# Kernel optimization log

Measured on AMD Instinct MI355X. Metric: run time of the kernel, lower is better.

Reference implementation:

```python
import jax, jax.numpy as jnp
import numpy as np
from jax import lax

B, IN_CH, OUT_CH, H, W = 32, 128, 256, 64, 64
STYLE_CH, TDIM, G = 512, 512, 32
GN_EPS, MOD_EPS = 1e-5, 1e-8
DN = ('NCHW', 'OIHW', 'NCHW')


def swish(x):
    return x * jax.nn.sigmoid(x)


def group_norm(x, gamma, beta):
    n, c, h, w = x.shape
    xr = x.reshape(n, G, c // G, h, w)
    mu = xr.mean(axis=(2, 3, 4), keepdims=True)
    var = xr.var(axis=(2, 3, 4), keepdims=True)
    xn = ((xr - mu) * lax.rsqrt(var + GN_EPS)).reshape(n, c, h, w)
    return xn * gamma[None, :, None, None] + beta[None, :, None, None]


def conv3x3(x, w, b):
    y = lax.conv_general_dilated(x, w, (1, 1), ((1, 1), (1, 1)), dimension_numbers=DN)
    return y + b[None, :, None, None]


def setup_inputs() -> dict:
    key = jax.random.key(0)
    ks = jax.random.split(key, 16)
    s = 0.05
    return {
        'x': jax.random.normal(ks[0], (B, IN_CH, H, W), jnp.float32),
        'temb': jax.random.normal(ks[1], (B, TDIM), jnp.float32),
        'style': jax.random.normal(ks[2], (B, STYLE_CH), jnp.float32),
        'gn1_g': jnp.ones((IN_CH,), jnp.float32),
        'gn1_b': jnp.zeros((IN_CH,), jnp.float32),
        'conv1_w': jax.random.normal(ks[3], (OUT_CH, IN_CH, 3, 3), jnp.float32) * s,
        'conv1_b': jnp.zeros((OUT_CH,), jnp.float32),
        'temb_w': jax.random.normal(ks[4], (OUT_CH, TDIM), jnp.float32) * s,
        'temb_b': jnp.zeros((OUT_CH,), jnp.float32),
        'gn2_g': jnp.ones((OUT_CH,), jnp.float32),
        'gn2_b': jnp.zeros((OUT_CH,), jnp.float32),
        'style_w': jax.random.normal(ks[5], (OUT_CH, STYLE_CH), jnp.float32) * s,
        'style_b': jnp.zeros((OUT_CH,), jnp.float32),
        'mod_w': jax.random.normal(ks[6], (OUT_CH, OUT_CH, 3, 3), jnp.float32) * s,
        'sc_w': jax.random.normal(ks[7], (OUT_CH, IN_CH, 1, 1), jnp.float32) * s,
        'sc_b': jnp.zeros((OUT_CH,), jnp.float32),
    }


def reference(x, temb, style, gn1_g, gn1_b, conv1_w, conv1_b, temb_w, temb_b,
              gn2_g, gn2_b, style_w, style_b, mod_w, sc_w, sc_b):
    # block1: GN -> Swish -> Conv3x3
    h = conv3x3(swish(group_norm(x, gn1_g, gn1_b)), conv1_w, conv1_b)
    # temb projection: Swish -> Linear, broadcast over HxW
    h = h + (swish(temb) @ temb_w.T + temb_b)[:, :, None, None]
    # block2: GN -> Swish -> Dropout(0) [identity]
    h = swish(group_norm(h, gn2_g, gn2_b))
    # modulated + demodulated per-sample conv (StyleGAN2-style)
    style2 = style @ style_w.T + style_b                       # (b, out_ch)
    wmod = mod_w[None] * (style2[:, None, :, None, None] + 1.0)  # (b, o, i, kh, kw)
    d = lax.rsqrt((wmod ** 2).sum(axis=(2, 3, 4), keepdims=True) + MOD_EPS)
    wmod = wmod * d
    conv1s = lambda xi, wi: lax.conv_general_dilated(
        xi[None], wi, (1, 1), ((1, 1), (1, 1)), dimension_numbers=DN)[0]
    h = jax.vmap(conv1s)(h, wmod)                              # per-sample conv
    # shortcut 1x1 conv (in_ch != out_ch)
    sc = lax.conv_general_dilated(x, sc_w, (1, 1), ((0, 0), (0, 0)), dimension_numbers=DN)
    sc = sc + sc_b[None, :, None, None]
    return h + sc
```

## Files before the change

kernel.cpp:

```cpp
#include <hip/hip_runtime.h>
#include <cstdint>

typedef unsigned short u16;
typedef unsigned int   u32;

typedef __attribute__((ext_vector_type(8))) short bf16x8;
typedef __attribute__((ext_vector_type(4))) float f32x4;

#define DEV __device__ __forceinline__

static constexpr int HP = 66, WP = 66;

DEV u16 f2bf(float f) {
  u32 u = __float_as_uint(f);
  u32 r = (u + 0x7fffu + ((u >> 16) & 1u)) >> 16;
  return (u16)r;
}
DEV float bf2f(u16 v) { return __uint_as_float((u32)v << 16); }

DEV void gload_lds16(const void* g, void* s) {
  __builtin_amdgcn_global_load_lds(
      (const __attribute__((address_space(1))) void*)g,
      (__attribute__((address_space(3))) void*)s, 16, 0, 0);
}

__global__ __launch_bounds__(256) void prep_kernel(const float* __restrict__ x,
                                                   const float* __restrict__ temb,
                                                   const float* __restrict__ temb_w,
                                                   const float* __restrict__ temb_b,
                                                   const float* __restrict__ conv1_b,
                                                   const float* __restrict__ style,
                                                   const float* __restrict__ style_w,
                                                   const float* __restrict__ style_b,
                                                   const float* __restrict__ conv1_w,
                                                   const float* __restrict__ mod_w,
                                                   float2* __restrict__ st1,
                                                   float* __restrict__ tb2,
                                                   float* __restrict__ mvec,
                                                   u16* __restrict__ w1T,
                                                   u16* __restrict__ wmT,
                                                   float* __restrict__ SS_T,
                                                   u16* __restrict__ act1p,
                                                   u16* __restrict__ act2p,
                                                   float* __restrict__ s2sum) {
  __shared__ float sh[512];
  int blk = blockIdx.x, t = threadIdx.x;
  if (blk < 1024) {
    const float4* p = (const float4*)(x + (size_t)blk * 16384);
    float s = 0.f, s2 = 0.f;
    for (int i = t; i < 4096; i += 256) {
      float4 v = p[i];
      s  += v.x + v.y + v.z + v.w;
      s2 += v.x*v.x + v.y*v.y + v.z*v.z + v.w*v.w;
    }
    for (int d = 32; d; d >>= 1) { s += __shfl_down(s, d); s2 += __shfl_down(s2, d); }
    if ((t & 63) == 0) { sh[t >> 6] = s; sh[4 + (t >> 6)] = s2; }
    __syncthreads();
    if (t == 0) {
      s  = sh[0] + sh[1] + sh[2] + sh[3];
      s2 = sh[4] + sh[5] + sh[6] + sh[7];
      float mean = s / 16384.f;
      float var  = s2 / 16384.f - mean * mean;
      st1[blk] = make_float2(mean, rsqrtf(var + 1e-5f));
    }
  } else if (blk < 1088) {
    int b2 = blk - 1024;
    if (b2 < 32) {
      int b = b2;
      for (int k = t; k < 512; k += 256) {
        float v = temb[b * 512 + k];
        sh[k] = v / (1.f + __expf(-v));
      }
      __syncthreads();
      const float4* wr = (const float4*)(temb_w + t * 512);
      float acc = 0.f;
      for (int k = 0; k < 128; ++k) {
        float4 w4 = wr[k];
        acc += w4.x * sh[k*4] + w4.y * sh[k*4+1] + w4.z * sh[k*4+2] + w4.w * sh[k*4+3];
      }
      tb2[b * 256 + t] = acc + temb_b[t] + conv1_b[t];
    } else {
      int b = b2 - 32;
      for (int k = t; k < 512; k += 256) sh[k] = style[b * 512 + k];
      __syncthreads();
      const float4* wr = (const float4*)(style_w + t * 512);
      float acc = 0.f;
      for (int k = 0; k < 128; ++k) {
        float4 w4 = wr[k];
        acc += w4.x * sh[k*4] + w4.y * sh[k*4+1] + w4.z * sh[k*4+2] + w4.w * sh[k*4+3];
      }
      mvec[b * 256 + t] = acc + style_b[t] + 1.f;
    }
  } else if (blk < 2240) {
    int idx = (blk - 1088) * 256 + t;
    int co = idx / 1152, r = idx - co * 1152;
    int s = r >> 7, ci = r & 127;
    int ky = s / 3, kx = s - ky * 3;
    w1T[idx] = f2bf(conv1_w[(co * 128 + ci) * 9 + ky * 3 + kx]);
  } else if (blk < 4544) {
    int idx = (blk - 2240) * 256 + t;
    int co = idx / 2304, r = idx - co * 2304;
    int s = r >> 8, ci = r & 255;
    int ky = s / 3, kx = s - ky * 3;
    wmT[idx] = f2bf(mod_w[(co * 256 + ci) * 9 + ky * 3 + kx]);
  } else if (blk < 4800) {
    int o = blk - 4544, i = t;
    const float* p = mod_w + (size_t)(o * 256 + i) * 9;
    float s = 0.f;
#pragma unroll
    for (int k = 0; k < 9; ++k) s += p[k] * p[k];
    SS_T[i * 256 + o] = s;
  } else if (blk < 6360) {
    bool big = blk >= 5320;
    int idx = (big ? (blk - 5320) : (blk - 4800)) * 256 + t;
    const int GR = big ? 32 : 16;
    int g = idx % GR;
    int p = (idx / GR) % 260;
    int b = idx / (GR * 260);
    int y, x2;
    if (p < 66)       { y = 0;       x2 = p; }
    else if (p < 132) { y = 65;      x2 = p - 66; }
    else if (p < 196) { y = p - 131; x2 = 0; }
    else              { y = p - 195; x2 = 65; }
    uint4 z; z.x = 0; z.y = 0; z.z = 0; z.w = 0;
    u16* buf = big ? act2p : act1p;
    int C = big ? 256 : 128;
    *(uint4*)(buf + (((size_t)b * HP + y) * WP + x2) * C + g * 8) = z;
  } else {
    *(float2*)(s2sum + t * 8)     = make_float2(0.f, 0.f);
    *(float2*)(s2sum + t * 8 + 2) = make_float2(0.f, 0.f);
    *(float2*)(s2sum + t * 8 + 4) = make_float2(0.f, 0.f);
    *(float2*)(s2sum + t * 8 + 6) = make_float2(0.f, 0.f);
  }
}

__global__ __launch_bounds__(256) void demod_sc_kernel(const float* __restrict__ mvec,
                                                       const float* __restrict__ SS_T,
                                                       const float* __restrict__ sc_w,
                                                       float* __restrict__ dvec,
                                                       u16* __restrict__ scTb) {
  __shared__ float m2[256];
  int b = blockIdx.x, t = threadIdx.x;
  float mv = mvec[b * 256 + t];
  m2[t] = mv * mv;
  __syncthreads();
  float acc = 0.f;
  for (int i = 0; i < 256; ++i) acc += m2[i] * SS_T[i * 256 + t];
  float X = acc + 1e-8f;
  dvec[b * 256 + t] = rsqrtf(X);
  float invd = sqrtf(X);
  const float4* wr = (const float4*)(sc_w + t * 128);
  u16* dst = scTb + ((size_t)b * 256 + t) * 128;
#pragma unroll 8
  for (int c4 = 0; c4 < 32; ++c4) {
    float4 w4 = wr[c4];
    u16 o[4] = { f2bf(w4.x * invd), f2bf(w4.y * invd),
                 f2bf(w4.z * invd), f2bf(w4.w * invd) };
    *(uint2*)(dst + c4 * 4) = *(const uint2*)o;
  }
}

__global__ __launch_bounds__(256) void gn1_apply_kernel(const float* __restrict__ x,
                                                        const float2* __restrict__ st1,
                                                        const float* __restrict__ g1,
                                                        const float* __restrict__ b1,
                                                        u16* __restrict__ act1p,
                                                        u16* __restrict__ xh) {
  __shared__ float xs[64][129];
  int blk = blockIdx.x;
  int b = blk >> 6, y = blk & 63;
  int t = threadIdx.x;
#pragma unroll
  for (int pass = 0; pass < 8; ++pass) {
    int c = pass * 16 + (t >> 4);
    int k = t & 15;
    float4 v = *(const float4*)(x + ((size_t)(b * 128 + c)) * 4096 + y * 64 + k * 4);
    xs[k * 4 + 0][c] = v.x;
    xs[k * 4 + 1][c] = v.y;
    xs[k * 4 + 2][c] = v.z;
    xs[k * 4 + 3][c] = v.w;
  }
  __syncthreads();
  const int cg = t & 15, c0 = cg * 8;
  float2 msA = st1[b * 32 + cg * 2];
  float2 msB = st1[b * 32 + cg * 2 + 1];
  float g1r[8], b1r[8];
#pragma unroll
  for (int e = 0; e < 8; ++e) { g1r[e] = g1[c0 + e]; b1r[e] = b1[c0 + e]; }
#pragma unroll
  for (int p = 0; p < 4; ++p) {
    int xi = p * 16 + (t >> 4);
    u16 outA[8], outX[8];
#pragma unroll
    for (int e = 0; e < 8; ++e) {
      float v = xs[xi][c0 + e];
      float2 ms = (e < 4) ? msA : msB;
      float vn = (v - ms.x) * ms.y * g1r[e] + b1r[e];
      float sw = vn / (1.f + __expf(-vn));
      outA[e] = f2bf(sw);
      outX[e] = f2bf(v);
    }
    *(uint4*)(act1p + (((size_t)b * HP + (y + 1)) * WP + (xi + 1)) * 128 + c0) =
        *(const uint4*)outA;
    *(uint4*)(xh + (((size_t)b * 64 + y) * 64 + xi) * 128 + c0) = *(const uint4*)outX;
  }
}

__global__ __launch_bounds__(256) void gn2_apply_kernel(const u16* __restrict__ h1,
                                                        const float* __restrict__ st2sum,
                                                        const float* __restrict__ g2,
                                                        const float* __restrict__ b2,
                                                        const float* __restrict__ mvec,
                                                        u16* __restrict__ act2p) {
  int idx = blockIdx.x * 256 + threadIdx.x;
  int gpix = idx >> 5;
  int gi = idx & 31;
  int c0 = gi * 8;
  int b = gpix >> 12, y = (gpix >> 6) & 63, x = gpix & 63;
  uint4 raw = *(const uint4*)(h1 + (size_t)gpix * 256 + c0);
  const u16* rs = (const u16*)&raw;
  float s  = st2sum[b * 64 + gi * 2];
  float s2 = st2sum[b * 64 + gi * 2 + 1];
  float mean = s / 32768.f;
  float rstd = rsqrtf(s2 / 32768.f - mean * mean + 1e-5f);
  const float* mv = mvec + b * 256 + c0;
  u16 outp[8];
#pragma unroll
  for (int e = 0; e < 8; ++e) {
    float v  = bf2f(rs[e]);
    float vn = (v - mean) * rstd * g2[c0 + e] + b2[c0 + e];
    float sw = vn / (1.f + __expf(-vn));
    outp[e] = f2bf(sw * mv[e]);
  }
  *(uint4*)(act2p + (((size_t)b * HP + (y + 1)) * WP + (x + 1)) * 256 + c0) = *(const uint4*)outp;
}

template <int MODE>
__global__ __launch_bounds__(512, 2) void igemm_kernel(const u16* __restrict__ act,
                                                       const u16* __restrict__ wT,
                                                       const float* __restrict__ epi,
                                                       const u16* __restrict__ xh,
                                                       const u16* __restrict__ scTb,
                                                       const float* __restrict__ sc_b,
                                                       u16* __restrict__ h1out,
                                                       float* __restrict__ fout,
                                                       float* __restrict__ st2sum) {
  constexpr int CIN    = (MODE == 0) ? 128 : 256;
  constexpr int KW     = CIN * 9;
  constexpr int NKMAIN = KW / 64;
  constexpr int NKT    = (MODE == 2) ? NKMAIN + 2 : NKMAIN;

  __shared__ __align__(16) unsigned char lds[131072];
  const int tid  = threadIdx.x;
  const int wave = tid >> 6, lane = tid & 63;
  const int wm = wave >> 2, wn = wave & 3;
  const int m_base = blockIdx.x * 256;
  const int bimg = m_base >> 12;
  const int ln = lane & 15, l4 = lane >> 4;

  const int srow = lane >> 3;
  const int glog = (lane & 7) ^ srow;

  u32 pixA[2][2], pixX[2][2], rowB[2][2], rowS[2][2];
#pragma unroll
  for (int j = 0; j < 2; ++j)
#pragma unroll
    for (int h = 0; h < 2; ++h) {
      int mlocal = (wave & 3) * 16 + j * 8 + srow + h * 64 + (wave >> 2) * 128;
      int m = m_base + mlocal;
      int y = (m >> 6) & 63, x = m & 63;
      pixA[j][h] = (u32)((bimg * HP + y) * WP + x) * CIN + glog * 8;
      if (MODE == 2) pixX[j][h] = (u32)m * 128 + glog * 8;
      int co = (wave >> 1) * 64 + h * 32 + (wave & 1) * 16 + j * 8 + srow;
      rowB[j][h] = (u32)co * KW + glog * 8;
      if (MODE == 2) rowS[j][h] = (u32)(bimg * 256 + co) * 128 + glog * 8;
    }

  f32x4 acc[8][4];
#pragma unroll
  for (int i = 0; i < 8; ++i)
#pragma unroll
    for (int j = 0; j < 4; ++j) acc[i][j] = (f32x4){0.f, 0.f, 0.f, 0.f};

  auto stageA = [&](int kt, int h, int buf) {
    unsigned char* dst = lds + buf * 65536 + h * 16384 + wave * 2048;
    if (MODE == 2 && kt >= NKMAIN) {
      u32 ko = (u32)(kt - NKMAIN) * 64;
      gload_lds16(xh + pixX[0][h] + ko, dst);
      gload_lds16(xh + pixX[1][h] + ko, dst + 1024);
    } else {
      int q = kt / 9;
      int tap = kt - q * 9;
      int kin = q * 64;
      int ky = tap / 3, kx = tap - ky * 3;
      u32 ko = (u32)((ky * WP + kx) * CIN + kin);
      gload_lds16(act + pixA[0][h] + ko, dst);
      gload_lds16(act + pixA[1][h] + ko, dst + 1024);
    }
  };
  auto stageB = [&](int kt, int g, int buf) {
    unsigned char* dst = lds + buf * 65536 + 32768 + g * 16384 + wave * 2048;
    if (MODE == 2 && kt >= NKMAIN) {
      u32 ko = (u32)(kt - NKMAIN) * 64;
      gload_lds16(scTb + rowS[0][g] + ko, dst);
      gload_lds16(scTb + rowS[1][g] + ko, dst + 1024);
    } else {
      int q = kt / 9;
      int tap = kt - q * 9;
      u32 ko = (u32)(tap * CIN + q * 64);
      gload_lds16(wT + rowB[0][g] + ko, dst);
      gload_lds16(wT + rowB[1][g] + ko, dst + 1024);
    }
  };

  bf16x8 af[8], bf[4];
  auto ldA = [&](int h, int buf) {
    const unsigned char* As = lds + buf * 65536;
#pragma unroll
    for (int f = 0; f < 4; ++f)
#pragma unroll
      for (int kk = 0; kk < 2; ++kk) {
        int lr = h * 128 + wm * 64 + f * 16 + ln;
        int gr = (kk * 4 + l4) ^ (lr & 7);
        af[f * 2 + kk] = *(const bf16x8*)(As + lr * 128 + gr * 16);
      }
  };
  auto ldB = [&](int g, int buf) {
    const unsigned char* Bs = lds + buf * 65536 + 32768;
#pragma unroll
    for (int f1 = 0; f1 < 2; ++f1)
#pragma unroll
      for (int kk = 0; kk < 2; ++kk) {
        int lr = g * 128 + wn * 32 + f1 * 16 + ln;
        int gr = (kk * 4 + l4) ^ (lr & 7);
        bf[f1 * 2 + kk] = *(const bf16x8*)(Bs + lr * 128 + gr * 16);
      }
  };
  auto mmac = [&](int h, int g) {
    __builtin_amdgcn_s_setprio(1);
#pragma unroll
    for (int f = 0; f < 4; ++f)
#pragma unroll
      for (int f1 = 0; f1 < 2; ++f1)
#pragma unroll
        for (int kk = 0; kk < 2; ++kk)
          acc[h * 4 + f][g * 2 + f1] = __builtin_amdgcn_mfma_f32_16x16x32_bf16(
              af[f * 2 + kk], bf[f1 * 2 + kk], acc[h * 4 + f][g * 2 + f1], 0, 0, 0);
    __builtin_amdgcn_s_setprio(0);
  };

#define PHASE_BAR() do { __builtin_amdgcn_sched_barrier(0); \
    __builtin_amdgcn_s_barrier(); __builtin_amdgcn_sched_barrier(0); } while (0)

  stageA(0, 0, 0); stageB(0, 0, 0); stageB(0, 1, 0); stageA(0, 1, 0);

#pragma unroll 2
  for (int kt = 0; kt < NKT - 1; ++kt) {
    const int cur = kt & 1, nxt = cur ^ 1;
    stageA(kt + 1, 0, nxt);
    asm volatile("s_waitcnt vmcnt(6)" ::: "memory");
    PHASE_BAR();
    ldB(0, cur); ldA(0, cur);
    mmac(0, 0);
    stageB(kt + 1, 0, nxt);
    asm volatile("s_waitcnt vmcnt(6)" ::: "memory");
    PHASE_BAR();
    ldB(1, cur);
    mmac(0, 1);
    stageB(kt + 1, 1, nxt);
    asm volatile("s_waitcnt vmcnt(6)" ::: "memory");
    PHASE_BAR();
    ldA(1, cur);
    mmac(1, 1);
    stageA(kt + 1, 1, nxt);
    PHASE_BAR();
    ldB(0, cur);
    mmac(1, 0);
  }
  {
    const int cur = (NKT - 1) & 1;
    asm volatile("s_waitcnt vmcnt(4)" ::: "memory");
    PHASE_BAR();
    ldB(0, cur); ldA(0, cur); mmac(0, 0);
    asm volatile("s_waitcnt vmcnt(2)" ::: "memory");
    PHASE_BAR();
    ldB(1, cur); mmac(0, 1);
    asm volatile("s_waitcnt vmcnt(0)" ::: "memory");
    PHASE_BAR();
    ldA(1, cur); mmac(1, 1);
    PHASE_BAR();
    ldB(0, cur); mmac(1, 0);
  }
#undef PHASE_BAR

  if (MODE == 0) {
    const float* tbrow = epi + bimg * 256;
    float ps[4], ps2[4];
#pragma unroll
    for (int fn = 0; fn < 4; ++fn) { ps[fn] = 0.f; ps2[fn] = 0.f; }
#pragma unroll
    for (int fm = 0; fm < 8; ++fm)
#pragma unroll
      for (int fn = 0; fn < 4; ++fn) {
        int co = wn * 64 + fn * 16 + ln;
        float add = tbrow[co];
#pragma unroll
        for (int i = 0; i < 4; ++i) {
          int m = m_base + wm * 128 + fm * 16 + (l4 << 2) + i;
          float v = acc[fm][fn][i] + add;
          h1out[(size_t)m * 256 + co] = f2bf(v);
          ps[fn] += v; ps2[fn] += v * v;
        }
      }
#pragma unroll
    for (int fn = 0; fn < 4; ++fn) {
      float s = ps[fn], s2 = ps2[fn];
      s += __shfl_xor(s, 1);  s2 += __shfl_xor(s2, 1);
      s += __shfl_xor(s, 2);  s2 += __shfl_xor(s2, 2);
      s += __shfl_xor(s, 4);  s2 += __shfl_xor(s2, 4);
      s += __shfl_xor(s, 16); s2 += __shfl_xor(s2, 16);
      s += __shfl_xor(s, 32); s2 += __shfl_xor(s2, 32);
      if ((lane & 55) == 0) {
        int g = wn * 8 + fn * 2 + (ln >> 3);
        atomicAdd(&st2sum[bimg * 64 + g * 2 + 0], s);
        atomicAdd(&st2sum[bimg * 64 + g * 2 + 1], s2);
      }
    }
  } else {
    float* tile = (float*)lds;
    const int pixb = m_base & 4095;
#pragma unroll
    for (int c = 0; c < 4; ++c) {
      __syncthreads();
      if (wn == c) {
#pragma unroll
        for (int fn = 0; fn < 4; ++fn) {
          int nl = fn * 16 + ln;
          int co = c * 64 + nl;
          float dsc = epi[bimg * 256 + co];
          float scb = sc_b[co];
#pragma unroll
          for (int fm = 0; fm < 8; ++fm)
#pragma unroll
            for (int i = 0; i < 4; ++i) {
              int ml = wm * 128 + fm * 16 + (l4 << 2) + i;
              tile[nl * 257 + ml] = acc[fm][fn][i] * dsc + scb;
            }
        }
      }
      __syncthreads();
#pragma unroll 4
      for (int it = 0; it < 32; ++it) {
        int lin = it * 512 + tid;
        int co_l = lin >> 8, ml = lin & 255;
        fout[((size_t)(bimg * 256 + c * 64 + co_l)) * 4096 + pixb + ml] =
            tile[co_l * 257 + ml];
      }
    }
  }
}

extern "C" void kernel_launch(void* const* d_in, const int* in_sizes, int n_in,
                              void* d_out, int out_size, void* d_ws, size_t ws_size,
                              hipStream_t stream) {
  const float* x       = (const float*)d_in[0];
  const float* temb    = (const float*)d_in[1];
  const float* style   = (const float*)d_in[2];
  const float* gn1_g   = (const float*)d_in[3];
  const float* gn1_b   = (const float*)d_in[4];
  const float* conv1_w = (const float*)d_in[5];
  const float* conv1_b = (const float*)d_in[6];
  const float* temb_w  = (const float*)d_in[7];
  const float* temb_b  = (const float*)d_in[8];
  const float* gn2_g   = (const float*)d_in[9];
  const float* gn2_b   = (const float*)d_in[10];
  const float* style_w = (const float*)d_in[11];
  const float* style_b = (const float*)d_in[12];
  const float* mod_w   = (const float*)d_in[13];
  const float* sc_w    = (const float*)d_in[14];
  const float* sc_b    = (const float*)d_in[15];
  float* out = (float*)d_out;
  char* ws = (char*)d_ws;

  size_t o = 0;
  auto alloc = [&](size_t bytes) { size_t r = o; o += (bytes + 255) & ~(size_t)255; return r; };
  const size_t act1p_bytes = (size_t)32 * HP * WP * 128 * 2;
  const size_t xh_bytes    = (size_t)32 * 64 * 64 * 128 * 2;
  const size_t h1_bytes    = (size_t)32 * 4096 * 256 * 2;
  const size_t act2p_bytes = (size_t)32 * HP * WP * 256 * 2;
  size_t o_act1p = alloc(act1p_bytes);
  size_t o_xh    = alloc(xh_bytes);
  size_t o_h1    = alloc(h1_bytes);
  size_t o_act2p = alloc(act2p_bytes);
  size_t o_w1T   = alloc((size_t)256 * 1152 * 2);
  size_t o_wmT   = alloc((size_t)256 * 2304 * 2);
  size_t o_scTb  = alloc((size_t)32 * 256 * 128 * 2);
  size_t o_tb2   = alloc(8192 * 4);
  size_t o_mvec  = alloc(8192 * 4);
  size_t o_dvec  = alloc(8192 * 4);
  size_t o_SS    = alloc((size_t)256 * 256 * 4);
  size_t o_st1   = alloc(1024 * 8);
  size_t o_s2sum = alloc(32 * 32 * 2 * 4);
  if (ws_size < o) return;

  u16*    act1p = (u16*)(ws + o_act1p);
  u16*    xh    = (u16*)(ws + o_xh);
  u16*    h1    = (u16*)(ws + o_h1);
  u16*    act2p = (u16*)(ws + o_act2p);
  u16*    w1T   = (u16*)(ws + o_w1T);
  u16*    wmT   = (u16*)(ws + o_wmT);
  u16*    scTb  = (u16*)(ws + o_scTb);
  float*  tb2   = (float*)(ws + o_tb2);
  float*  mvec  = (float*)(ws + o_mvec);
  float*  dvec  = (float*)(ws + o_dvec);
  float*  SS_T  = (float*)(ws + o_SS);
  float2* st1   = (float2*)(ws + o_st1);
  float*  s2sum = (float*)(ws + o_s2sum);

  prep_kernel<<<6361, 256, 0, stream>>>(x, temb, temb_w, temb_b, conv1_b,
                                        style, style_w, style_b, conv1_w, mod_w,
                                        st1, tb2, mvec, w1T, wmT, SS_T,
                                        act1p, act2p, s2sum);
  gn1_apply_kernel<<<2048, 256, 0, stream>>>(x, st1, gn1_g, gn1_b, act1p, xh);
  demod_sc_kernel<<<32, 256, 0, stream>>>(mvec, SS_T, sc_w, dvec, scTb);

  igemm_kernel<0><<<512, 512, 0, stream>>>(act1p, w1T, tb2, nullptr, nullptr,
                                           nullptr, h1, nullptr, s2sum);

  gn2_apply_kernel<<<16384, 256, 0, stream>>>(h1, s2sum, gn2_g, gn2_b, mvec, act2p);

  igemm_kernel<2><<<512, 512, 0, stream>>>(act2p, wmT, dvec, xh, scTb,
                                           sc_b, nullptr, out, nullptr);
}
```

Before: 335.2 us.

## Reorder GEMM main loop so LDS reads issue before barrier

Restructures the software-pipelined conv GEMM main loop so each phase issues its LDS fragment reads first, then the next global-to-LDS stage and vmcnt wait, then the barrier and an lgkmcnt wait before the MFMAs. The separate epilogue iteration is folded into the loop with a 'more' predicate. The intent is to overlap LDS read latency with global-load issue and the barrier, rather than serializing barrier then reads then math. Because buffers are overwritten across phases, the correctness of the new wait counts and the barrier placement is delicate.

```diff
diff --git a/kernel.cpp b/kernel.cpp
--- a/kernel.cpp
+++ b/kernel.cpp
@@ -349,49 +349,45 @@
     __builtin_amdgcn_s_setprio(0);
   };
 
-#define PHASE_BAR() do { __builtin_amdgcn_sched_barrier(0); \
-    __builtin_amdgcn_s_barrier(); __builtin_amdgcn_sched_barrier(0); } while (0)
+#define SB() __builtin_amdgcn_sched_barrier(0)
+#define LGKM0() asm volatile("s_waitcnt lgkmcnt(0)" ::: "memory")
 
   stageA(0, 0, 0); stageB(0, 0, 0); stageB(0, 1, 0); stageA(0, 1, 0);
+  asm volatile("s_waitcnt vmcnt(4)" ::: "memory");
+  __builtin_amdgcn_s_barrier();
 
 #pragma unroll 2
-  for (int kt = 0; kt < NKT - 1; ++kt) {
+  for (int kt = 0; kt < NKT; ++kt) {
     const int cur = kt & 1, nxt = cur ^ 1;
-    stageA(kt + 1, 0, nxt);
-    asm volatile("s_waitcnt vmcnt(6)" ::: "memory");
-    PHASE_BAR();
-    ldB(0, cur); ldA(0, cur);
+    const bool more = (kt + 1 < NKT);
+    ldB(0, cur); ldA(0, cur); SB();
+    if (more) { stageA(kt + 1, 0, nxt);
+                asm volatile("s_waitcnt vmcnt(4)" ::: "memory"); }
+    else      { asm volatile("s_waitcnt vmcnt(2)" ::: "memory"); }
+    __builtin_amdgcn_s_barrier();
+    LGKM0(); SB();
     mmac(0, 0);
-    stageB(kt + 1, 0, nxt);
-    asm volatile("s_waitcnt vmcnt(6)" ::: "memory");
-    PHASE_BAR();
-    ldB(1, cur);
+    ldB(1, cur); SB();
+    if (more) { stageB(kt + 1, 0, nxt);
+                asm volatile("s_waitcnt vmcnt(4)" ::: "memory"); }
+    else      { asm volatile("s_waitcnt vmcnt(0)" ::: "memory"); }
+    __builtin_amdgcn_s_barrier();
+    LGKM0(); SB();
     mmac(0, 1);
-    stageB(kt + 1, 1, nxt);
-    asm volatile("s_waitcnt vmcnt(6)" ::: "memory");
-    PHASE_BAR();
-    ldA(1, cur);
+    ldA(1, cur); SB();
+    if (more) stageB(kt + 1, 1, nxt);
+    __builtin_amdgcn_s_barrier();
+    LGKM0(); SB();
     mmac(1, 1);
-    stageA(kt + 1, 1, nxt);
-    PHASE_BAR();
-    ldB(0, cur);
+    ldB(0, cur); SB();
+    if (more) { stageA(kt + 1, 1, nxt);
+                asm volatile("s_waitcnt vmcnt(4)" ::: "memory"); }
+    __builtin_amdgcn_s_barrier();
+    LGKM0(); SB();
     mmac(1, 0);
   }
-  {
-    const int cur = (NKT - 1) & 1;
-    asm volatile("s_waitcnt vmcnt(4)" ::: "memory");
-    PHASE_BAR();
-    ldB(0, cur); ldA(0, cur); mmac(0, 0);
-    asm volatile("s_waitcnt vmcnt(2)" ::: "memory");
-    PHASE_BAR();
-    ldB(1, cur); mmac(0, 1);
-    asm volatile("s_waitcnt vmcnt(0)" ::: "memory");
-    PHASE_BAR();
-    ldA(1, cur); mmac(1, 1);
-    PHASE_BAR();
-    ldB(0, cur); mmac(1, 0);
-  }
-#undef PHASE_BAR
+#undef SB
+#undef LGKM0
 
   if (MODE == 0) {
     const float* tbrow = epi + bimg * 256;
```

New measurement: 607.4 us. 1.81x slower.
